# Performance work log

Measured on AMD Instinct MI355X. Metric: run time of the kernel, lower is better.

Reference implementation:

```python
import jax, jax.numpy as jnp
import numpy as np

D_MODEL = 1024
N_HEADS = 16
D_HEAD = D_MODEL // N_HEADS
ROPE_BASE = 10000.0
B, L = 2, 2048


def setup_inputs() -> dict:
    key = jax.random.key(0)
    k1, k2, k3 = jax.random.split(key, 3)
    x = jax.random.normal(k1, (B, L, D_MODEL), dtype=jnp.float32)
    W_qkv = jax.random.normal(k2, (3 * D_MODEL, D_MODEL), dtype=jnp.float32) * (1.0 / np.sqrt(D_MODEL))
    W_out = jax.random.normal(k3, (D_MODEL, D_MODEL), dtype=jnp.float32) * (1.0 / np.sqrt(D_MODEL))
    position_ids = jnp.broadcast_to(jnp.arange(L, dtype=jnp.int32), (B, L))
    attn_mask_2d = jnp.broadcast_to(jnp.tril(jnp.ones((L, L), dtype=bool)), (B, L, L))
    return {"x": x, "W_qkv": W_qkv, "W_out": W_out,
            "position_ids": position_ids, "attn_mask_2d": attn_mask_2d}


def _apply_rope(t, position_ids, inv_freq):
    # t: (B, H, L, Dh) float32; position_ids: (B, L) int
    f = position_ids.astype(jnp.float32)[:, :, None] * inv_freq  # (B, L, Dh/2)
    cos = jnp.cos(f)[:, None]  # (B, 1, L, Dh/2)
    sin = jnp.sin(f)[:, None]
    x1 = t[..., 0::2]
    x2 = t[..., 1::2]
    rot_even = x1 * cos - x2 * sin
    rot_odd = x1 * sin + x2 * cos
    return jnp.stack((rot_even, rot_odd), axis=-1).reshape(t.shape)


def reference(x, W_qkv, W_out, position_ids, attn_mask_2d):
    Bb, Ll, D = x.shape
    H, Dh = N_HEADS, D // N_HEADS
    inv_freq = 1.0 / (ROPE_BASE ** (jnp.arange(0, Dh, 2, dtype=jnp.float32) / Dh))  # (Dh/2,)
    qkv = jnp.einsum('bld,ed->ble', x, W_qkv).reshape(Bb, Ll, 3, H, Dh)
    qkv = jnp.transpose(qkv, (2, 0, 3, 1, 4))  # (3, B, H, L, Dh)
    q, k, v = qkv[0], qkv[1], qkv[2]
    q = _apply_rope(q.astype(jnp.float32), position_ids, inv_freq).astype(x.dtype)
    k = _apply_rope(k.astype(jnp.float32), position_ids, inv_freq).astype(x.dtype)
    scale = 1.0 / np.sqrt(Dh).astype(np.float32)
    scores = jnp.einsum('bhld,bhmd->bhlm', q, k) * scale  # (B, H, L, L)
    neg = jnp.finfo(scores.dtype).min
    scores = jnp.where(attn_mask_2d[:, None], scores, neg)
    attn = jax.nn.softmax(scores, axis=-1)
    out = jnp.einsum('bhlm,bhmd->bhld', attn, v)
    out = jnp.transpose(out, (0, 2, 1, 3)).reshape(Bb, Ll, D)
    return jnp.einsum('bld,ed->ble', out, W_out)
```

## Files before the change

kernel.cpp:

```cpp
#include <hip/hip_runtime.h>
#include <hip/hip_bf16.h>
#include <math.h>

typedef float f32x4 __attribute__((ext_vector_type(4)));
typedef __bf16 bf16x8 __attribute__((ext_vector_type(8)));

__device__ inline f32x4 mfma16(bf16x8 a, bf16x8 b, f32x4 c) {
    return __builtin_amdgcn_mfma_f32_16x16x32_bf16(a, b, c, 0, 0, 0);
}
__device__ inline unsigned short f2bf(float f) {
    union { float f; unsigned u; } v; v.f = f;
    unsigned r = v.u + 0x7fffu + ((v.u >> 16) & 1u);
    return (unsigned short)(r >> 16);
}
__device__ inline float bf2f(unsigned short b) {
    union { unsigned u; float f; } v; v.u = ((unsigned)b) << 16;
    return v.f;
}
__device__ inline unsigned pack2(float a, float b) {
    return (unsigned)f2bf(a) | ((unsigned)f2bf(b) << 16);
}
__device__ inline f32x4 vzero() { f32x4 z = {0.f, 0.f, 0.f, 0.f}; return z; }

#define GLD16(gptr, lptr)                                                            \
    __builtin_amdgcn_global_load_lds(                                                \
        (const __attribute__((address_space(1))) unsigned int*)(const void*)(gptr),  \
        (__attribute__((address_space(3))) unsigned int*)(void*)(lptr), 16, 0, 0)

__global__ __launch_bounds__(256)
void convert_xw(const float* __restrict__ x, const float* __restrict__ wqkv,
                unsigned short* __restrict__ xb, unsigned short* __restrict__ wqkvb)
{
    int i = blockIdx.x * 256 + threadIdx.x;
    const float* src; unsigned short* dst; int off;
    if (i < 524288) { src = x;    dst = xb;    off = i; }
    else            { src = wqkv; dst = wqkvb; off = i - 524288; }
    const float4* p = (const float4*)src + (size_t)off * 2;
    float4 f0 = p[0], f1 = p[1];
    uint4 o;
    o.x = pack2(f0.x, f0.y); o.y = pack2(f0.z, f0.w);
    o.z = pack2(f1.x, f1.y); o.w = pack2(f1.z, f1.w);
    ((uint4*)dst)[off] = o;
}

template<int MI, int C32, int WPB>
__global__ __launch_bounds__(256, WPB)
void gemm_bt(const unsigned short* __restrict__ A,
             const unsigned short* __restrict__ Wt,
             void* __restrict__ C_, int M, int N, int K)
{
    __shared__ __align__(16) unsigned short As[MI * 32 * 64];
    __shared__ __align__(16) unsigned short Bs[128 * 64];

    const int tid  = threadIdx.x;
    const int wave = tid >> 6;
    const int lane = tid & 63;
    const int quad = lane >> 4;
    const int c0   = lane & 15;
    const int m0 = blockIdx.y * (MI * 32);
    const int n0 = blockIdx.x * 128;
    const int wm = (wave >> 1) * (MI * 16);
    const int wn = (wave & 1) * 64;

    const int lrow   = lane >> 3;
    const int gchunk = (lane & 7) ^ lrow;
    const int goff   = gchunk * 8;

    f32x4 acc[MI][4];
#pragma unroll
    for (int i = 0; i < MI; i++)
#pragma unroll
        for (int j = 0; j < 4; j++) acc[i][j] = vzero();

    for (int k0 = 0; k0 < K; k0 += 64) {
        __syncthreads();
#pragma unroll
        for (int p = 0; p < MI; p++) {
            int r0 = p * 32 + wave * 8;
            GLD16(&A[(size_t)(m0 + r0 + lrow) * K + k0 + goff], &As[r0 * 64]);
        }
#pragma unroll
        for (int p = 0; p < 4; p++) {
            int r0 = p * 32 + wave * 8;
            GLD16(&Wt[(size_t)(n0 + r0 + lrow) * K + k0 + goff], &Bs[r0 * 64]);
        }
        __syncthreads();
#pragma unroll
        for (int kk = 0; kk < 2; kk++) {
            const int pos = ((kk * 4 + quad) ^ (c0 & 7)) * 8;
            bf16x8 af[MI], bfr[4];
#pragma unroll
            for (int i = 0; i < MI; i++)
                af[i] = *(const bf16x8*)&As[(wm + i * 16 + c0) * 64 + pos];
#pragma unroll
            for (int j = 0; j < 4; j++)
                bfr[j] = *(const bf16x8*)&Bs[(wn + j * 16 + c0) * 64 + pos];
#pragma unroll
            for (int i = 0; i < MI; i++)
#pragma unroll
                for (int j = 0; j < 4; j++)
                    acc[i][j] = mfma16(af[i], bfr[j], acc[i][j]);
        }
    }

#pragma unroll
    for (int i = 0; i < MI; i++)
#pragma unroll
        for (int j = 0; j < 4; j++)
#pragma unroll
            for (int r = 0; r < 4; r++) {
                int row  = m0 + wm + i * 16 + quad * 4 + r;
                int colg = n0 + wn + j * 16 + c0;
                if (C32) ((float*)C_)[(size_t)row * N + colg] = acc[i][j][r];
                else ((unsigned short*)C_)[(size_t)row * N + colg] = f2bf(acc[i][j][r]);
            }
}

__global__ __launch_bounds__(256)
void rope_vtrans(const unsigned short* __restrict__ qkv,
                 const int* __restrict__ pos,
                 unsigned short* __restrict__ Qb,
                 unsigned short* __restrict__ Kb,
                 unsigned short* __restrict__ Vt,
                 const float* __restrict__ wout,
                 unsigned short* __restrict__ woutb)
{
    __shared__ unsigned short T[256 * 64];
    const int id = blockIdx.x;
    if (id < 8192) {
        int tid = id * 256 + threadIdx.x;
        int d2 = tid & 31;
        int h  = (tid >> 5) & 15;
        int l  = (tid >> 9) & 2047;
        int b  = tid >> 20;
        size_t row = (size_t)(b * 2048 + l) * 3072;
        int col = h * 64 + 2 * d2;
        float inv_freq = exp2f((float)(-2 * d2) * (13.287712379549449f / 64.0f));
        float f = (float)pos[b * 2048 + l] * inv_freq;
        float s, c;
        sincosf(f, &s, &c);
        unsigned qw = *(const unsigned*)&qkv[row + col];
        unsigned kw = *(const unsigned*)&qkv[row + 1024 + col];
        float q1 = bf2f((unsigned short)qw), q2 = bf2f((unsigned short)(qw >> 16));
        float k1 = bf2f((unsigned short)kw), k2 = bf2f((unsigned short)(kw >> 16));
        const float qs = 0.18033688011112042f;
        size_t o = ((size_t)((b * 16 + h) * 2048 + l)) * 64 + 2 * d2;
        *(unsigned*)&Qb[o] = pack2((q1 * c - q2 * s) * qs, (q1 * s + q2 * c) * qs);
        *(unsigned*)&Kb[o] = pack2(k1 * c - k2 * s, k1 * s + k2 * c);
    } else if (id < 8448) {
        const int id2 = id - 8192;
        const int t = threadIdx.x;
        const int l0 = (id2 & 7) * 256, h = (id2 >> 3) & 15, b = id2 >> 7;
#pragma unroll
        for (int i = 0; i < 8; i++) {
            int c = t + i * 256;
            int r = c >> 3, c8 = c & 7;
            int p = (c8 + (r >> 3)) & 7;
            *(uint4*)&T[r * 64 + p * 8] =
                *(const uint4*)&qkv[(size_t)(b * 2048 + l0 + r) * 3072 + 2048 + h * 64 + c8 * 8];
        }
        __syncthreads();
#pragma unroll
        for (int i = 0; i < 8; i++) {
            int c = t + i * 256;
            int dh = c >> 5, lc = c & 31;
            int blk = dh >> 3;
            unsigned short tmp[8];
#pragma unroll
            for (int j = 0; j < 8; j++) {
                int l = lc * 8 + j;
                int p = (blk + lc) & 7;
                tmp[j] = T[l * 64 + p * 8 + (dh & 7)];
            }
            *(uint4*)&Vt[((size_t)(b * 16 + h) * 64 + dh) * 2048 + l0 + lc * 8] = *(uint4*)tmp;
        }
    } else {
        int i = (id - 8448) * 256 + threadIdx.x;
        const float4* p = (const float4*)wout + (size_t)i * 2;
        float4 f0 = p[0], f1 = p[1];
        uint4 o;
        o.x = pack2(f0.x, f0.y); o.y = pack2(f0.z, f0.w);
        o.z = pack2(f1.x, f1.y); o.w = pack2(f1.z, f1.w);
        ((uint4*)woutb)[i] = o;
    }
}

__global__ __launch_bounds__(256, 2)
void attn(const unsigned short* __restrict__ Q,
          const unsigned short* __restrict__ Kb,
          const unsigned short* __restrict__ Vt,
          unsigned short* __restrict__ O)
{
    __shared__ unsigned short Ks2[2][64 * 64];
    __shared__ unsigned short Vts2[2][64 * 64];
    __shared__ unsigned short PsA[64 * 64];
    __shared__ unsigned short PsB[64 * 64];

    const int tid  = threadIdx.x;
    const int wave = tid >> 6;
    const int lane = tid & 63;
    const int quad = lane >> 4;
    const int c0   = lane & 15;
    const int id = blockIdx.x;
    const int jp = id >> 5;
    const int h  = id & 15;
    const int b  = (id >> 4) & 1;
    const int qtA = jp, qtB = 31 - jp;
    const size_t headoff = ((size_t)(b * 16 + h)) * 2048 * 64;
    const int q0A = qtA * 64, q0B = qtB * 64;
    const float C = 11.541560327111707f;

    const int ca = tid, cb2 = tid + 256;
    const int ra = ca >> 3, c8a = ca & 7;
    const int rb = cb2 >> 3, c8b = cb2 & 7;
    const int la = ra * 64 + (c8a ^ (ra & 7)) * 8;
    const int lb = rb * 64 + (c8b ^ (rb & 7)) * 8;

    const int qrow = wave * 16 + c0;
    const int psrow = qrow * 64;
    const int xsw = (c0 & 7) << 3;

    bf16x8 ones;
#pragma unroll
    for (int j = 0; j < 8; j++) ones[j] = (__bf16)1.0f;

    const size_t qbaseA = headoff + (size_t)(q0A + wave * 16 + c0) * 64;
    const size_t qbaseB = headoff + (size_t)(q0B + wave * 16 + c0) * 64;
    bf16x8 aqA0 = *(const bf16x8*)&Q[qbaseA + quad * 8];
    bf16x8 aqA1 = *(const bf16x8*)&Q[qbaseA + (4 + quad) * 8];
    bf16x8 aqB0 = *(const bf16x8*)&Q[qbaseB + quad * 8];
    bf16x8 aqB1 = *(const bf16x8*)&Q[qbaseB + (4 + quad) * 8];

    uint4 kE0 = *(const uint4*)&Kb[headoff + (size_t)ra * 64 + c8a * 8];
    uint4 kE1 = *(const uint4*)&Kb[headoff + (size_t)rb * 64 + c8b * 8];
    uint4 vE0 = *(const uint4*)&Vt[headoff + (size_t)ra * 2048 + c8a * 8];
    uint4 vE1 = *(const uint4*)&Vt[headoff + (size_t)rb * 2048 + c8b * 8];
    uint4 kO0 = *(const uint4*)&Kb[headoff + 4096 + (size_t)ra * 64 + c8a * 8];
    uint4 kO1 = *(const uint4*)&Kb[headoff + 4096 + (size_t)rb * 64 + c8b * 8];
    uint4 vO0 = *(const uint4*)&Vt[headoff + (size_t)ra * 2048 + 64 + c8a * 8];
    uint4 vO1 = *(const uint4*)&Vt[headoff + (size_t)rb * 2048 + 64 + c8b * 8];

    f32x4 oA[4], oB[4];
#pragma unroll
    for (int j = 0; j < 4; j++) { oA[j] = vzero(); oB[j] = vzero(); }
    f32x4 laccA = vzero(), laccB = vzero();

    auto chunk_compute = [&](const unsigned short* KsC, const unsigned short* VtsC,
                             int kc) {
        {
            f32x4 s[4];
#pragma unroll
            for (int nj = 0; nj < 4; nj++) s[nj] = vzero();
            __builtin_amdgcn_s_setprio(1);
#pragma unroll
            for (int kk = 0; kk < 2; kk++) {
                const int pos = ((kk * 4 + quad) ^ (c0 & 7)) * 8;
                bf16x8 aq = kk ? aqB1 : aqB0;
#pragma unroll
                for (int nj = 0; nj < 4; nj++) {
                    bf16x8 bk = *(const bf16x8*)&KsC[(nj * 16 + c0) * 64 + pos];
                    s[nj] = mfma16(bk, aq, s[nj]);
                }
            }
            __builtin_amdgcn_s_setprio(0);
            if (kc == qtB) {
#pragma unroll
                for (int nj = 0; nj < 4; nj++)
#pragma unroll
                    for (int r = 0; r < 4; r++) {
                        int key = nj * 16 + quad * 4 + r;
                        if (key > qrow) s[nj][r] = -1e38f;
                    }
            }
#pragma unroll
            for (int nj = 0; nj < 4; nj++) {
                unsigned u0, u1, u2, u3;
                { union { float f; unsigned u; } pv; pv.f = __builtin_amdgcn_exp2f(s[nj][0] - C); u0 = pv.u; }
                { union { float f; unsigned u; } pv; pv.f = __builtin_amdgcn_exp2f(s[nj][1] - C); u1 = pv.u; }
                { union { float f; unsigned u; } pv; pv.f = __builtin_amdgcn_exp2f(s[nj][2] - C); u2 = pv.u; }
                { union { float f; unsigned u; } pv; pv.f = __builtin_amdgcn_exp2f(s[nj][3] - C); u3 = pv.u; }
                uint2 w;
                w.x = (u0 >> 16) | (u1 & 0xffff0000u);
                w.y = (u2 >> 16) | (u3 & 0xffff0000u);
                *(uint2*)&PsB[psrow + ((nj * 16 + quad * 4) ^ xsw)] = w;
            }
        }
        if (kc <= qtA) {
            f32x4 s[4];
#pragma unroll
            for (int nj = 0; nj < 4; nj++) s[nj] = vzero();
            __builtin_amdgcn_s_setprio(1);
#pragma unroll
            for (int kk = 0; kk < 2; kk++) {
                const int pos = ((kk * 4 + quad) ^ (c0 & 7)) * 8;
                bf16x8 aq = kk ? aqA1 : aqA0;
#pragma unroll
                for (int nj = 0; nj < 4; nj++) {
                    bf16x8 bk = *(const bf16x8*)&KsC[(nj * 16 + c0) * 64 + pos];
                    s[nj] = mfma16(bk, aq, s[nj]);
                }
            }
            __builtin_amdgcn_s_setprio(0);
            if (kc == qtA) {
#pragma unroll
                for (int nj = 0; nj < 4; nj++)
#pragma unroll
                    for (int r = 0; r < 4; r++) {
                        int key = nj * 16 + quad * 4 + r;
                        if (key > qrow) s[nj][r] = -1e38f;
                    }
            }
#pragma unroll
            for (int nj = 0; nj < 4; nj++) {
                unsigned u0, u1, u2, u3;
                { union { float f; unsigned u; } pv; pv.f = __builtin_amdgcn_exp2f(s[nj][0] - C); u0 = pv.u; }
                { union { float f; unsigned u; } pv; pv.f = __builtin_amdgcn_exp2f(s[nj][1] - C); u1 = pv.u; }
                { union { float f; unsigned u; } pv; pv.f = __builtin_amdgcn_exp2f(s[nj][2] - C); u2 = pv.u; }
                { union { float f; unsigned u; } pv; pv.f = __builtin_amdgcn_exp2f(s[nj][3] - C); u3 = pv.u; }
                uint2 w;
                w.x = (u0 >> 16) | (u1 & 0xffff0000u);
                w.y = (u2 >> 16) | (u3 & 0xffff0000u);
                *(uint2*)&PsA[psrow + ((nj * 16 + quad * 4) ^ xsw)] = w;
            }
        }
        asm volatile("s_waitcnt lgkmcnt(0)" ::: "memory");

        __builtin_amdgcn_s_setprio(1);
#pragma unroll
        for (int kk = 0; kk < 2; kk++) {
            const int pos = ((kk * 4 + quad) ^ (c0 & 7)) * 8;
            bf16x8 ap = *(const bf16x8*)&PsB[psrow + ((kk * 32 + quad * 8) ^ xsw)];
            laccB = mfma16(ap, ones, laccB);
#pragma unroll
            for (int cj = 0; cj < 4; cj++) {
                bf16x8 bv = *(const bf16x8*)&VtsC[(cj * 16 + c0) * 64 + pos];
                oB[cj] = mfma16(ap, bv, oB[cj]);
            }
        }
        __builtin_amdgcn_s_setprio(0);
        if (kc <= qtA) {
            __builtin_amdgcn_s_setprio(1);
#pragma unroll
            for (int kk = 0; kk < 2; kk++) {
                const int pos = ((kk * 4 + quad) ^ (c0 & 7)) * 8;
                bf16x8 ap = *(const bf16x8*)&PsA[psrow + ((kk * 32 + quad * 8) ^ xsw)];
                laccA = mfma16(ap, ones, laccA);
#pragma unroll
                for (int cj = 0; cj < 4; cj++) {
                    bf16x8 bv = *(const bf16x8*)&VtsC[(cj * 16 + c0) * 64 + pos];
                    oA[cj] = mfma16(ap, bv, oA[cj]);
                }
            }
            __builtin_amdgcn_s_setprio(0);
        }
    };

    const int nkv = (qtB >> 1) + 1;
    for (int kt2 = 0; kt2 < nkv; kt2++) {
        const int ce = 2 * kt2, co = ce + 1;
        const bool hasOdd = (co <= qtB);
        __syncthreads();
        *(uint4*)&Ks2[0][la] = kE0;
        *(uint4*)&Ks2[0][lb] = kE1;
        *(uint4*)&Vts2[0][la] = vE0;
        *(uint4*)&Vts2[0][lb] = vE1;
        if (hasOdd) {
            *(uint4*)&Ks2[1][la] = kO0;
            *(uint4*)&Ks2[1][lb] = kO1;
            *(uint4*)&Vts2[1][la] = vO0;
            *(uint4*)&Vts2[1][lb] = vO1;
        }
        __syncthreads();
        if (kt2 + 1 < nkv) {
            const int ne = ce + 2, no = ce + 3;
            size_t k1o = headoff + (size_t)ne * 4096;
            kE0 = *(const uint4*)&Kb[k1o + (size_t)ra * 64 + c8a * 8];
            kE1 = *(const uint4*)&Kb[k1o + (size_t)rb * 64 + c8b * 8];
            vE0 = *(const uint4*)&Vt[headoff + (size_t)ra * 2048 + ne * 64 + c8a * 8];
            vE1 = *(const uint4*)&Vt[headoff + (size_t)rb * 2048 + ne * 64 + c8b * 8];
            if (no <= qtB) {
                size_t k2o = headoff + (size_t)no * 4096;
                kO0 = *(const uint4*)&Kb[k2o + (size_t)ra * 64 + c8a * 8];
                kO1 = *(const uint4*)&Kb[k2o + (size_t)rb * 64 + c8b * 8];
                vO0 = *(const uint4*)&Vt[headoff + (size_t)ra * 2048 + no * 64 + c8a * 8];
                vO1 = *(const uint4*)&Vt[headoff + (size_t)rb * 2048 + no * 64 + c8b * 8];
            }
        }
        chunk_compute(Ks2[0], Vts2[0], ce);
        if (hasOdd) chunk_compute(Ks2[1], Vts2[1], co);
    }

#pragma unroll
    for (int r = 0; r < 4; r++) {
        float invA = 1.0f / laccA[r];
        float invB = 1.0f / laccB[r];
        int qlA = q0A + wave * 16 + quad * 4 + r;
        int qlB = q0B + wave * 16 + quad * 4 + r;
        size_t baseA = ((size_t)b * 2048 + qlA) * 1024 + h * 64;
        size_t baseB = ((size_t)b * 2048 + qlB) * 1024 + h * 64;
#pragma unroll
        for (int cj = 0; cj < 4; cj++) {
            O[baseA + cj * 16 + c0] = f2bf(oA[cj][r] * invA);
            O[baseB + cj * 16 + c0] = f2bf(oB[cj][r] * invB);
        }
    }
}

extern "C" void kernel_launch(void* const* d_in, const int* in_sizes, int n_in,
                              void* d_out, int out_size, void* d_ws, size_t ws_size,
                              hipStream_t stream) {
    const int* pos = (const int*)d_in[3];

    unsigned short* regA = (unsigned short*)d_ws;
    unsigned short* regB = regA + (size_t)4096 * 1024;
    unsigned short* regC = regB + (size_t)4096 * 1024;
    unsigned short* regD = regC + (size_t)4096 * 1024;
    unsigned short* regE = regD + (size_t)4096 * 3072;

    unsigned short* xb    = regA;
    unsigned short* wqkvb = regB;
    unsigned short* qkv   = regD;
    unsigned short* Qb    = regA;
    unsigned short* Kb    = regB;
    unsigned short* Vt    = regC;
    unsigned short* Ob    = regD;
    unsigned short* woutb = regE;

    convert_xw<<<3584, 256, 0, stream>>>((const float*)d_in[0], (const float*)d_in[1],
                                         xb, wqkvb);
    gemm_bt<4, 0, 4><<<dim3(24, 32), 256, 0, stream>>>(xb, wqkvb, qkv, 4096, 3072, 1024);
    rope_vtrans<<<8960, 256, 0, stream>>>(qkv, pos, Qb, Kb, Vt,
                                          (const float*)d_in[2], woutb);
    attn<<<512, 256, 0, stream>>>(Qb, Kb, Vt, Ob);
    gemm_bt<2, 1, 3><<<dim3(8, 64), 256, 0, stream>>>(Ob, woutb, d_out, 4096, 1024, 1024);
}
```

Baseline: 193.1 us.

## Batch QK^T for even/odd chunks before PV and share RoPE sincos per row

The attention loop is split into separate score (s_tile) and PV (pv_tile) phases. Scores for both the even and odd KV chunks, for both query tiles, are computed first into four separate P buffers, followed by a single LDS wait, and only then are all the PV MFMAs issued. This cuts the number of lgkmcnt waits per iteration and gives longer independent MFMA streams, at the cost of 16KB more LDS, which may affect occupancy. Separately, the RoPE kernel now computes sincos once per (b,l) row in shared memory instead of once per thread, which adds a block-wide barrier.

Measured after the change: 193.4 us (median of 2 runs). Within noise of the previous version (+0.2%).

```diff
diff --git a/kernel.cpp b/kernel.cpp
--- a/kernel.cpp
+++ b/kernel.cpp
@@ -126,19 +126,26 @@
                  unsigned short* __restrict__ woutb)
 {
     __shared__ unsigned short T[256 * 64];
+    __shared__ float2 SC[32];
     const int id = blockIdx.x;
     if (id < 8192) {
-        int tid = id * 256 + threadIdx.x;
+        int t = threadIdx.x;
+        int tid = id * 256 + t;
+        int l  = (tid >> 9) & 2047;
+        int b  = tid >> 20;
+        if (t < 32) {
+            float inv_freq = exp2f((float)(-2 * t) * (13.287712379549449f / 64.0f));
+            float f = (float)pos[b * 2048 + l] * inv_freq;
+            float s, c;
+            sincosf(f, &s, &c);
+            SC[t] = make_float2(s, c);
+        }
+        __syncthreads();
         int d2 = tid & 31;
         int h  = (tid >> 5) & 15;
-        int l  = (tid >> 9) & 2047;
-        int b  = tid >> 20;
+        float s = SC[d2].x, c = SC[d2].y;
         size_t row = (size_t)(b * 2048 + l) * 3072;
         int col = h * 64 + 2 * d2;
-        float inv_freq = exp2f((float)(-2 * d2) * (13.287712379549449f / 64.0f));
-        float f = (float)pos[b * 2048 + l] * inv_freq;
-        float s, c;
-        sincosf(f, &s, &c);
         unsigned qw = *(const unsigned*)&qkv[row + col];
         unsigned kw = *(const unsigned*)&qkv[row + 1024 + col];
         float q1 = bf2f((unsigned short)qw), q2 = bf2f((unsigned short)(qw >> 16));
@@ -193,8 +200,10 @@
 {
     __shared__ unsigned short Ks2[2][64 * 64];
     __shared__ unsigned short Vts2[2][64 * 64];
-    __shared__ unsigned short PsA[64 * 64];
-    __shared__ unsigned short PsB[64 * 64];
+    __shared__ unsigned short PsBe[64 * 64];
+    __shared__ unsigned short PsAe[64 * 64];
+    __shared__ unsigned short PsBo[64 * 64];
+    __shared__ unsigned short PsAo[64 * 64];
 
     const int tid  = threadIdx.x;
     const int wave = tid >> 6;
@@ -245,120 +254,67 @@
     for (int j = 0; j < 4; j++) { oA[j] = vzero(); oB[j] = vzero(); }
     f32x4 laccA = vzero(), laccB = vzero();
 
-    auto chunk_compute = [&](const unsigned short* KsC, const unsigned short* VtsC,
-                             int kc) {
-        {
-            f32x4 s[4];
-#pragma unroll
-            for (int nj = 0; nj < 4; nj++) s[nj] = vzero();
-            __builtin_amdgcn_s_setprio(1);
-#pragma unroll
-            for (int kk = 0; kk < 2; kk++) {
-                const int pos = ((kk * 4 + quad) ^ (c0 & 7)) * 8;
-                bf16x8 aq = kk ? aqB1 : aqB0;
-#pragma unroll
-                for (int nj = 0; nj < 4; nj++) {
-                    bf16x8 bk = *(const bf16x8*)&KsC[(nj * 16 + c0) * 64 + pos];
-                    s[nj] = mfma16(bk, aq, s[nj]);
-                }
-            }
-            __builtin_amdgcn_s_setprio(0);
-            if (kc == qtB) {
-#pragma unroll
-                for (int nj = 0; nj < 4; nj++)
-#pragma unroll
-                    for (int r = 0; r < 4; r++) {
-                        int key = nj * 16 + quad * 4 + r;
-                        if (key > qrow) s[nj][r] = -1e38f;
-                    }
-            }
-#pragma unroll
-            for (int nj = 0; nj < 4; nj++) {
-                unsigned u0, u1, u2, u3;
-                { union { float f; unsigned u; } pv; pv.f = __builtin_amdgcn_exp2f(s[nj][0] - C); u0 = pv.u; }
-                { union { float f; unsigned u; } pv; pv.f = __builtin_amdgcn_exp2f(s[nj][1] - C); u1 = pv.u; }
-                { union { float f; unsigned u; } pv; pv.f = __builtin_amdgcn_exp2f(s[nj][2] - C); u2 = pv.u; }
-                { union { float f; unsigned u; } pv; pv.f = __builtin_amdgcn_exp2f(s[nj][3] - C); u3 = pv.u; }
-                uint2 w;
-                w.x = (u0 >> 16) | (u1 & 0xffff0000u);
-                w.y = (u2 >> 16) | (u3 & 0xffff0000u);
-                *(uint2*)&PsB[psrow + ((nj * 16 + quad * 4) ^ xsw)] = w;
-            }
-        }
-        if (kc <= qtA) {
-            f32x4 s[4];
-#pragma unroll
-            for (int nj = 0; nj < 4; nj++) s[nj] = vzero();
-            __builtin_amdgcn_s_setprio(1);
-#pragma unroll
-            for (int kk = 0; kk < 2; kk++) {
-                const int pos = ((kk * 4 + quad) ^ (c0 & 7)) * 8;
-                bf16x8 aq = kk ? aqA1 : aqA0;
-#pragma unroll
-                for (int nj = 0; nj < 4; nj++) {
-                    bf16x8 bk = *(const bf16x8*)&KsC[(nj * 16 + c0) * 64 + pos];
-                    s[nj] = mfma16(bk, aq, s[nj]);
-                }
-            }
-            __builtin_amdgcn_s_setprio(0);
-            if (kc == qtA) {
-#pragma unroll
-                for (int nj = 0; nj < 4; nj++)
-#pragma unroll
-                    for (int r = 0; r < 4; r++) {
-                        int key = nj * 16 + quad * 4 + r;
-                        if (key > qrow) s[nj][r] = -1e38f;
-                    }
-            }
-#pragma unroll
-            for (int nj = 0; nj < 4; nj++) {
-                unsigned u0, u1, u2, u3;
-                { union { float f; unsigned u; } pv; pv.f = __builtin_amdgcn_exp2f(s[nj][0] - C); u0 = pv.u; }
-                { union { float f; unsigned u; } pv; pv.f = __builtin_amdgcn_exp2f(s[nj][1] - C); u1 = pv.u; }
-                { union { float f; unsigned u; } pv; pv.f = __builtin_amdgcn_exp2f(s[nj][2] - C); u2 = pv.u; }
-                { union { float f; unsigned u; } pv; pv.f = __builtin_amdgcn_exp2f(s[nj][3] - C); u3 = pv.u; }
-                uint2 w;
-                w.x = (u0 >> 16) | (u1 & 0xffff0000u);
-                w.y = (u2 >> 16) | (u3 & 0xffff0000u);
-                *(uint2*)&PsA[psrow + ((nj * 16 + quad * 4) ^ xsw)] = w;
-            }
-        }
-        asm volatile("s_waitcnt lgkmcnt(0)" ::: "memory");
-
+    auto s_tile = [&](const unsigned short* KsC, unsigned short* Ps,
+                      bf16x8 aq0, bf16x8 aq1, int kc, int qt) {
+        f32x4 s[4];
+#pragma unroll
+        for (int nj = 0; nj < 4; nj++) s[nj] = vzero();
         __builtin_amdgcn_s_setprio(1);
 #pragma unroll
         for (int kk = 0; kk < 2; kk++) {
             const int pos = ((kk * 4 + quad) ^ (c0 & 7)) * 8;
-            bf16x8 ap = *(const bf16x8*)&PsB[psrow + ((kk * 32 + quad * 8) ^ xsw)];
-            laccB = mfma16(ap, ones, laccB);
+            bf16x8 aq = kk ? aq1 : aq0;
+#pragma unroll
+            for (int nj = 0; nj < 4; nj++) {
+                bf16x8 bk = *(const bf16x8*)&KsC[(nj * 16 + c0) * 64 + pos];
+                s[nj] = mfma16(bk, aq, s[nj]);
+            }
+        }
+        __builtin_amdgcn_s_setprio(0);
+        if (kc == qt) {
+#pragma unroll
+            for (int nj = 0; nj < 4; nj++)
+#pragma unroll
+                for (int r = 0; r < 4; r++) {
+                    int key = nj * 16 + quad * 4 + r;
+                    if (key > qrow) s[nj][r] = -1e38f;
+                }
+        }
+#pragma unroll
+        for (int nj = 0; nj < 4; nj++) {
+            unsigned u0, u1, u2, u3;
+            { union { float f; unsigned u; } pv; pv.f = __builtin_amdgcn_exp2f(s[nj][0] - C); u0 = pv.u; }
+            { union { float f; unsigned u; } pv; pv.f = __builtin_amdgcn_exp2f(s[nj][1] - C); u1 = pv.u; }
+            { union { float f; unsigned u; } pv; pv.f = __builtin_amdgcn_exp2f(s[nj][2] - C); u2 = pv.u; }
+            { union { float f; unsigned u; } pv; pv.f = __builtin_amdgcn_exp2f(s[nj][3] - C); u3 = pv.u; }
+            uint2 w;
+            w.x = (u0 >> 16) | (u1 & 0xffff0000u);
+            w.y = (u2 >> 16) | (u3 & 0xffff0000u);
+            *(uint2*)&Ps[psrow + ((nj * 16 + quad * 4) ^ xsw)] = w;
+        }
+    };
+    auto pv_tile = [&](const unsigned short* VtsC, const unsigned short* Ps,
+                       f32x4* o, f32x4& lacc) {
+        __builtin_amdgcn_s_setprio(1);
+#pragma unroll
+        for (int kk = 0; kk < 2; kk++) {
+            const int pos = ((kk * 4 + quad) ^ (c0 & 7)) * 8;
+            bf16x8 ap = *(const bf16x8*)&Ps[psrow + ((kk * 32 + quad * 8) ^ xsw)];
+            lacc = mfma16(ap, ones, lacc);
 #pragma unroll
             for (int cj = 0; cj < 4; cj++) {
                 bf16x8 bv = *(const bf16x8*)&VtsC[(cj * 16 + c0) * 64 + pos];
-                oB[cj] = mfma16(ap, bv, oB[cj]);
+                o[cj] = mfma16(ap, bv, o[cj]);
             }
         }
         __builtin_amdgcn_s_setprio(0);
-        if (kc <= qtA) {
-            __builtin_amdgcn_s_setprio(1);
-#pragma unroll
-            for (int kk = 0; kk < 2; kk++) {
-                const int pos = ((kk * 4 + quad) ^ (c0 & 7)) * 8;
-                bf16x8 ap = *(const bf16x8*)&PsA[psrow + ((kk * 32 + quad * 8) ^ xsw)];
-                laccA = mfma16(ap, ones, laccA);
-#pragma unroll
-                for (int cj = 0; cj < 4; cj++) {
-                    bf16x8 bv = *(const bf16x8*)&VtsC[(cj * 16 + c0) * 64 + pos];
-                    oA[cj] = mfma16(ap, bv, oA[cj]);
-                }
-            }
-            __builtin_amdgcn_s_setprio(0);
-        }
     };
 
     const int nkv = (qtB >> 1) + 1;
     for (int kt2 = 0; kt2 < nkv; kt2++) {
         const int ce = 2 * kt2, co = ce + 1;
         const bool hasOdd = (co <= qtB);
+        const bool doAe = (ce <= qtA), doAo = (co <= qtA);
         __syncthreads();
         *(uint4*)&Ks2[0][la] = kE0;
         *(uint4*)&Ks2[0][lb] = kE1;
@@ -386,8 +342,21 @@
                 vO1 = *(const uint4*)&Vt[headoff + (size_t)rb * 2048 + no * 64 + c8b * 8];
             }
         }
-        chunk_compute(Ks2[0], Vts2[0], ce);
-        if (hasOdd) chunk_compute(Ks2[1], Vts2[1], co);
+
+        s_tile(Ks2[0], PsBe, aqB0, aqB1, ce, qtB);
+        if (doAe) s_tile(Ks2[0], PsAe, aqA0, aqA1, ce, qtA);
+        if (hasOdd) {
+            s_tile(Ks2[1], PsBo, aqB0, aqB1, co, qtB);
+            if (doAo) s_tile(Ks2[1], PsAo, aqA0, aqA1, co, qtA);
+        }
+        asm volatile("s_waitcnt lgkmcnt(0)" ::: "memory");
+
+        pv_tile(Vts2[0], PsBe, oB, laccB);
+        if (doAe) pv_tile(Vts2[0], PsAe, oA, laccA);
+        if (hasOdd) {
+            pv_tile(Vts2[1], PsBo, oB, laccB);
+            if (doAo) pv_tile(Vts2[1], PsAo, oA, laccA);
+        }
     }
 
 #pragma unroll
```
